# Kernel optimization log

Measured on AMD Instinct MI355X. Metric: run time of the kernel, lower is better.

## Reference

```python
import jax, jax.numpy as jnp
import numpy as np


def setup_inputs() -> dict:
    key = jax.random.key(0)
    k1, k2, k3, k4, k5 = jax.random.split(key, 5)
    B, S, E, U = 32, 2048, 1024, 1024
    last_hidden_state = jax.random.normal(k1, (B, S, E), dtype=jnp.float32)
    attention_mask = jax.random.randint(k2, (B, S), 0, 2, dtype=jnp.int32)
    # ensure at least one valid token per row to avoid all -inf softmax
    attention_mask = attention_mask.at[:, 0].set(1)
    W = jax.random.normal(k3, (U, E), dtype=jnp.float32) * (E ** -0.5)
    Umat = jax.random.normal(k4, (U, E), dtype=jnp.float32) * (E ** -0.5)
    v = jax.random.normal(k5, (1, U), dtype=jnp.float32) * (U ** -0.5)
    return {"last_hidden_state": last_hidden_state, "attention_mask": attention_mask,
            "W": W, "U": Umat, "v": v}


def reference(last_hidden_state, attention_mask, W, U, v):
    # last_hidden_state: [B,S,E]; W,U: [units,E]; v: [1,units]
    Q = jnp.einsum('bse,ue->bsu', last_hidden_state, W)
    K = jnp.einsum('bse,ue->bsu', last_hidden_state, U)
    H = jnp.tanh(Q + K)                                   # [B,S,units]
    E = jnp.einsum('bsu,ou->bso', H, v)                   # [B,S,1]
    neg_inf = jnp.array(-jnp.inf, dtype=E.dtype)
    E = jnp.where(attention_mask[:, :, None] == 0, neg_inf, E)
    alpha = jax.nn.softmax(E, axis=1)                     # softmax over seq dim
    return jnp.sum(alpha * last_hidden_state, axis=1)     # [B,E]
```

## Files before the change

kernel.cpp:

```cpp
#include <hip/hip_runtime.h>
#include <hip/hip_bf16.h>


typedef short bf16x8 __attribute__((ext_vector_type(8)));
typedef float f32x4  __attribute__((ext_vector_type(4)));
typedef unsigned short u16x8 __attribute__((ext_vector_type(8)));

static __device__ __forceinline__ unsigned short f2bf(float f) {
    unsigned int x = __float_as_uint(f);
    unsigned int r = x + 0x7FFFu + ((x >> 16) & 1u);
    return (unsigned short)(r >> 16);
}

static __device__ __forceinline__ float fast_tanh(float x) {
    float e = __builtin_amdgcn_exp2f(x * 2.885390082f);
    float r = __builtin_amdgcn_rcpf(e + 1.0f);
    return __builtin_fmaf(-2.0f, r, 1.0f);
}

__global__ __launch_bounds__(256)
void prep_index(const float* __restrict__ W, const float* __restrict__ U,
                const int* __restrict__ mask,
                unsigned short* __restrict__ wsum,
                float* __restrict__ score, float* __restrict__ out,
                unsigned short* __restrict__ ridx, int* __restrict__ cnt) {
    __shared__ int sc[256];
    int blk = blockIdx.x, t = threadIdx.x;
    if (blk < 1024) {
        int g = blk * 256 + t;
        int i4 = g * 4;
        float4 w = *(const float4*)&W[i4];
        float4 u = *(const float4*)&U[i4];
        ushort4 h;
        h.x = f2bf(w.x + u.x); h.y = f2bf(w.y + u.y);
        h.z = f2bf(w.z + u.z); h.w = f2bf(w.w + u.w);
        *(ushort4*)&wsum[i4] = h;
        if (g < 65536) score[g] = 0.0f;
        if (g < 32768) out[g] = 0.0f;
    } else {
        int b = blk - 1024;
        const int* mrow = mask + b * 2048;
        int m[8], c = 0;
#pragma unroll
        for (int j = 0; j < 8; ++j) { m[j] = mrow[t * 8 + j]; c += (m[j] != 0); }
        sc[t] = c;
        __syncthreads();
        for (int off = 1; off < 256; off <<= 1) {
            int v = (t >= off) ? sc[t - off] : 0;
            __syncthreads();
            sc[t] += v;
            __syncthreads();
        }
        int base = sc[t] - c;
        unsigned short* rb = ridx + b * 2048;
#pragma unroll
        for (int j = 0; j < 8; ++j)
            if (m[j]) rb[base++] = (unsigned short)(t * 8 + j);
        if (t == 255) cnt[b] = sc[255];
    }
}

__global__ __launch_bounds__(256)
void gather_convert(const float* __restrict__ lhs, const unsigned short* __restrict__ ridx,
                    const int* __restrict__ cnt, unsigned short* __restrict__ Ab) {
    int b = blockIdx.y;
    int c = cnt[b];
    int cpad = (c + 127) & ~127;
    int r = blockIdx.x * 4 + (threadIdx.x >> 6);
    int lt = threadIdx.x & 63;
    if (r >= cpad) return;
    unsigned short* dst = Ab + ((size_t)b * 2048 + r) * 1024 + lt * 16;
    if (r < c) {
        int s = ridx[b * 2048 + r];
        const float* src = lhs + ((size_t)b * 2048 + s) * 1024 + lt * 16;
        float4 a0 = *(const float4*)(src + 0);
        float4 a1 = *(const float4*)(src + 4);
        float4 a2 = *(const float4*)(src + 8);
        float4 a3 = *(const float4*)(src + 12);
        u16x8 h0, h1;
        h0[0] = f2bf(a0.x); h0[1] = f2bf(a0.y); h0[2] = f2bf(a0.z); h0[3] = f2bf(a0.w);
        h0[4] = f2bf(a1.x); h0[5] = f2bf(a1.y); h0[6] = f2bf(a1.z); h0[7] = f2bf(a1.w);
        h1[0] = f2bf(a2.x); h1[1] = f2bf(a2.y); h1[2] = f2bf(a2.z); h1[3] = f2bf(a2.w);
        h1[4] = f2bf(a3.x); h1[5] = f2bf(a3.y); h1[6] = f2bf(a3.z); h1[7] = f2bf(a3.w);
        *(u16x8*)(dst + 0) = h0;
        *(u16x8*)(dst + 8) = h1;
    } else {
        u16x8 z = (u16x8){0,0,0,0,0,0,0,0};
        *(u16x8*)(dst + 0) = z;
        *(u16x8*)(dst + 8) = z;
    }
}

__global__ __launch_bounds__(256)
void score_gemm_bf16(const unsigned short* __restrict__ Ab,
                     const unsigned short* __restrict__ Bw,
                     const float* __restrict__ v, const int* __restrict__ cnt,
                     float* __restrict__ score) {
    const int K = 1024;
    __shared__ __align__(16) unsigned short As[128 * 64];
    __shared__ __align__(16) unsigned short Bs[128 * 64];

    const int bid    = (int)blockIdx.x;
    const int group  = bid >> 6;
    const int mt     = (group << 3) + (bid & 7);
    const int nI     = (bid >> 3) & 7;
    const int b      = mt >> 4;
    const int lm0    = (mt & 15) << 7;
    const int c      = cnt[b];
    if (lm0 >= ((c + 127) & ~127)) return;
    const int m0     = (b << 11) + lm0;
    const int n0     = nI << 7;

    const int t    = threadIdx.x;
    const int lane = t & 63;
    const int wave = t >> 6;
    const int wm   = (wave & 1) * 64;
    const int wn   = (wave >> 1) * 64;
    const int ml   = lane & 15;
    const int q    = lane >> 4;
    const int xorv = ml & 7;

    f32x4 acc[4][4];
#pragma unroll
    for (int i = 0; i < 4; ++i)
#pragma unroll
        for (int j = 0; j < 4; ++j)
            acc[i][j] = (f32x4){0.f, 0.f, 0.f, 0.f};

    const unsigned short* gA[4];
    const unsigned short* gB[4];
    unsigned short* lA[4];
    unsigned short* lB[4];
#pragma unroll
    for (int p = 0; p < 4; ++p) {
        int l   = p * 256 + wave * 64 + lane;
        int row = l >> 3;
        int kc  = (l & 7) ^ (row & 7);
        gA[p] = Ab + (size_t)(m0 + row) * K + kc * 8;
        gB[p] = Bw + (size_t)(n0 + row) * K + kc * 8;
        lA[p] = &As[(p * 4 + wave) * 512];
        lB[p] = &Bs[(p * 4 + wave) * 512];
    }

    for (int kk = 0; kk < K; kk += 64) {
#pragma unroll
        for (int p = 0; p < 4; ++p) {
            __builtin_amdgcn_global_load_lds((const __attribute__((address_space(1))) unsigned int*)gA[p],
                                             (__attribute__((address_space(3))) unsigned int*)lA[p], 16, 0, 0);
            __builtin_amdgcn_global_load_lds((const __attribute__((address_space(1))) unsigned int*)gB[p],
                                             (__attribute__((address_space(3))) unsigned int*)lB[p], 16, 0, 0);
            gA[p] += 64; gB[p] += 64;
        }
        __syncthreads();

#pragma unroll
        for (int s = 0; s < 2; ++s) {
            const int koff = ((s * 4 + q) ^ xorv) * 8;
            bf16x8 af[4], bf[4];
#pragma unroll
            for (int i = 0; i < 4; ++i)
                af[i] = *(const bf16x8*)&As[(wm + i * 16 + ml) * 64 + koff];
#pragma unroll
            for (int j = 0; j < 4; ++j)
                bf[j] = *(const bf16x8*)&Bs[(wn + j * 16 + ml) * 64 + koff];
#pragma unroll
            for (int i = 0; i < 4; ++i)
#pragma unroll
                for (int j = 0; j < 4; ++j)
                    acc[i][j] = __builtin_amdgcn_mfma_f32_16x16x32_bf16(af[i], bf[j], acc[i][j], 0, 0, 0);
        }
        __syncthreads();
    }

    float vw[4];
#pragma unroll
    for (int j = 0; j < 4; ++j)
        vw[j] = v[n0 + wn + j * 16 + ml];

#pragma unroll
    for (int i = 0; i < 4; ++i) {
#pragma unroll
        for (int r = 0; r < 4; ++r) {
            float val = 0.f;
#pragma unroll
            for (int j = 0; j < 4; ++j)
                val += fast_tanh(acc[i][j][r]) * vw[j];
#pragma unroll
            for (int off = 8; off > 0; off >>= 1)
                val += __shfl_xor(val, off, 64);
            if (ml == 0)
                atomicAdd(&score[m0 + wm + i * 16 + q * 4 + r], val);
        }
    }
}

__global__ __launch_bounds__(256)
void softmax_compact(const float* __restrict__ score, const int* __restrict__ cnt,
                     float* __restrict__ alphac) {
    int b = blockIdx.x, t = threadIdx.x;
    int c = cnt[b];
    __shared__ float red[8];
    float sc[8];
    float mx = -1e30f;
#pragma unroll
    for (int i = 0; i < 8; ++i) {
        int k = i * 256 + t;
        sc[i] = (k < c) ? score[b * 2048 + k] : -1e30f;
        mx = fmaxf(mx, sc[i]);
    }
#pragma unroll
    for (int off = 32; off > 0; off >>= 1)
        mx = fmaxf(mx, __shfl_xor(mx, off, 64));
    if ((t & 63) == 0) red[t >> 6] = mx;
    __syncthreads();
    mx = fmaxf(fmaxf(red[0], red[1]), fmaxf(red[2], red[3]));
    float e[8], sum = 0.f;
#pragma unroll
    for (int i = 0; i < 8; ++i) {
        int k = i * 256 + t;
        e[i] = (k < c) ? __expf(sc[i] - mx) : 0.f;
        sum += e[i];
    }
#pragma unroll
    for (int off = 32; off > 0; off >>= 1)
        sum += __shfl_xor(sum, off, 64);
    if ((t & 63) == 0) red[4 + (t >> 6)] = sum;
    __syncthreads();
    float inv = 1.0f / (red[4] + red[5] + red[6] + red[7]);
#pragma unroll
    for (int i = 0; i < 8; ++i) {
        int k = i * 256 + t;
        if (k < c) alphac[b * 2048 + k] = e[i] * inv;
    }
}

__global__ __launch_bounds__(256)
void wsum_bf16(const unsigned short* __restrict__ Ab, const float* __restrict__ alphac,
               const int* __restrict__ cnt, float* __restrict__ out) {
    int b   = blockIdx.x >> 4;
    int seg = blockIdx.x & 15;
    int t   = threadIdx.x;
    int c   = cnt[b];
    int per = (c + 15) >> 4;
    int s0  = seg * per;
    int s1  = min(s0 + per, c);
    const float* ap = alphac + b * 2048;
    const unsigned short* base = Ab + (size_t)b * 2048 * 1024 + t * 4;
    float a0 = 0.f, a1 = 0.f, a2 = 0.f, a3 = 0.f;
    for (int s = s0; s < s1; ++s) {
        float a = ap[s];
        ushort4 h = *(const ushort4*)(base + (size_t)s * 1024);
        a0 = __builtin_fmaf(a, __uint_as_float((unsigned)h.x << 16), a0);
        a1 = __builtin_fmaf(a, __uint_as_float((unsigned)h.y << 16), a1);
        a2 = __builtin_fmaf(a, __uint_as_float((unsigned)h.z << 16), a2);
        a3 = __builtin_fmaf(a, __uint_as_float((unsigned)h.w << 16), a3);
    }
    float* o = out + b * 1024 + t * 4;
    atomicAdd(o + 0, a0);
    atomicAdd(o + 1, a1);
    atomicAdd(o + 2, a2);
    atomicAdd(o + 3, a3);
}

#define LDSS 40
__global__ __launch_bounds__(256)
void score_gemm_f32stage(const float* __restrict__ A, const unsigned short* __restrict__ Bw,
                         const float* __restrict__ v, float* __restrict__ score) {
    const int K = 1024;
    __shared__ __align__(16) unsigned short As[128][LDSS];
    __shared__ __align__(16) unsigned short Bs[128][LDSS];
    const int n0 = (int)blockIdx.x * 128;
    const int m0 = (int)blockIdx.y * 128;
    const int t = threadIdx.x, lane = t & 63, wave = t >> 6;
    const int wm = (wave & 1) * 64, wn = (wave >> 1) * 64;
    const int ml = lane & 15, q = lane >> 4;
    f32x4 acc[4][4];
#pragma unroll
    for (int i = 0; i < 4; ++i)
#pragma unroll
        for (int j = 0; j < 4; ++j) acc[i][j] = (f32x4){0.f,0.f,0.f,0.f};
    const int sr = t >> 3, sc = (t & 7) * 4;
    for (int kk = 0; kk < K; kk += 32) {
#pragma unroll
        for (int p = 0; p < 4; ++p) {
            int r = sr + p * 32;
            float4 va = *(const float4*)&A[(size_t)(m0 + r) * K + kk + sc];
            ushort4 h; h.x = f2bf(va.x); h.y = f2bf(va.y); h.z = f2bf(va.z); h.w = f2bf(va.w);
            *(ushort4*)&As[r][sc] = h;
            ushort4 vb = *(const ushort4*)&Bw[(size_t)(n0 + r) * K + kk + sc];
            *(ushort4*)&Bs[r][sc] = vb;
        }
        __syncthreads();
        bf16x8 af[4], bf[4];
#pragma unroll
        for (int i = 0; i < 4; ++i) af[i] = *(const bf16x8*)&As[wm + i * 16 + ml][q * 8];
#pragma unroll
        for (int j = 0; j < 4; ++j) bf[j] = *(const bf16x8*)&Bs[wn + j * 16 + ml][q * 8];
#pragma unroll
        for (int i = 0; i < 4; ++i)
#pragma unroll
            for (int j = 0; j < 4; ++j)
                acc[i][j] = __builtin_amdgcn_mfma_f32_16x16x32_bf16(af[i], bf[j], acc[i][j], 0, 0, 0);
        __syncthreads();
    }
    float vw[4];
#pragma unroll
    for (int j = 0; j < 4; ++j) vw[j] = v[n0 + wn + j * 16 + ml];
#pragma unroll
    for (int i = 0; i < 4; ++i)
#pragma unroll
        for (int r = 0; r < 4; ++r) {
            float val = 0.f;
#pragma unroll
            for (int j = 0; j < 4; ++j) val += fast_tanh(acc[i][j][r]) * vw[j];
#pragma unroll
            for (int off = 8; off > 0; off >>= 1) val += __shfl_xor(val, off, 64);
            if (ml == 0) atomicAdd(&score[m0 + wm + i * 16 + q * 4 + r], val);
        }
}

__global__ __launch_bounds__(256)
void softmax_kernel(const float* __restrict__ score, const int* __restrict__ mask,
                    float* __restrict__ alpha) {
    const int S = 2048;
    int b = blockIdx.x, t = threadIdx.x;
    __shared__ float red[8];
    float sc[8]; int vd[8];
    float mx = -1e30f;
#pragma unroll
    for (int i = 0; i < 8; ++i) {
        int s = i * 256 + t;
        vd[i] = mask[b * S + s];
        sc[i] = score[b * S + s];
        if (vd[i]) mx = fmaxf(mx, sc[i]);
    }
#pragma unroll
    for (int off = 32; off > 0; off >>= 1)
        mx = fmaxf(mx, __shfl_xor(mx, off, 64));
    if ((t & 63) == 0) red[t >> 6] = mx;
    __syncthreads();
    mx = fmaxf(fmaxf(red[0], red[1]), fmaxf(red[2], red[3]));
    float e[8]; float sum = 0.f;
#pragma unroll
    for (int i = 0; i < 8; ++i) {
        e[i] = vd[i] ? __expf(sc[i] - mx) : 0.f;
        sum += e[i];
    }
#pragma unroll
    for (int off = 32; off > 0; off >>= 1)
        sum += __shfl_xor(sum, off, 64);
    if ((t & 63) == 0) red[4 + (t >> 6)] = sum;
    __syncthreads();
    float inv = 1.0f / (red[4] + red[5] + red[6] + red[7]);
#pragma unroll
    for (int i = 0; i < 8; ++i)
        alpha[b * S + i * 256 + t] = e[i] * inv;
}

__global__ __launch_bounds__(256)
void wsum_kernel(const float* __restrict__ lhs, const float* __restrict__ alpha,
                 float* __restrict__ out) {
    const int S = 2048, E = 1024;
    int b = blockIdx.x >> 6;
    int seg = blockIdx.x & 63;
    int t = threadIdx.x;
    int s0 = seg * 32;
    const float* base = lhs + ((size_t)b * S + s0) * E + t * 4;
    const float* ap = alpha + b * S + s0;
    float4 acc = {0.f, 0.f, 0.f, 0.f};
#pragma unroll 4
    for (int s = 0; s < 32; ++s) {
        float a = ap[s];
        if (a != 0.f) {
            float4 x = *(const float4*)(base + (size_t)s * E);
            acc.x += a * x.x; acc.y += a * x.y; acc.z += a * x.z; acc.w += a * x.w;
        }
    }
    float* o = out + b * E + t * 4;
    atomicAdd(o + 0, acc.x);
    atomicAdd(o + 1, acc.y);
    atomicAdd(o + 2, acc.z);
    atomicAdd(o + 3, acc.w);
}

extern "C" void kernel_launch(void* const* d_in, const int* in_sizes, int n_in,
                              void* d_out, int out_size, void* d_ws, size_t ws_size,
                              hipStream_t stream) {
    const float* lhs  = (const float*)d_in[0];
    const int*   mask = (const int*)d_in[1];
    const float* W    = (const float*)d_in[2];
    const float* Um   = (const float*)d_in[3];
    const float* v    = (const float*)d_in[4];
    float* out = (float*)d_out;

    char* ws = (char*)d_ws;
    unsigned short* wsum  = (unsigned short*)ws;
    float* score          = (float*)(ws + 2048u * 1024u);
    float* alphac         = (float*)(ws + 2304u * 1024u);
    unsigned short* ridx  = (unsigned short*)(ws + 2560u * 1024u);
    int* cnt              = (int*)(ws + 2688u * 1024u);
    unsigned short* Ab    = (unsigned short*)(ws + 2816u * 1024u);
    const size_t need = 2816ull * 1024ull + 131072ull * 1024ull;

    prep_index<<<1056, 256, 0, stream>>>(W, Um, mask, wsum, score, out, ridx, cnt);
    if (ws_size >= need) {
        dim3 gg(512, 32);
        gather_convert<<<gg, 256, 0, stream>>>(lhs, ridx, cnt, Ab);
        score_gemm_bf16<<<4096, 256, 0, stream>>>(Ab, wsum, v, cnt, score);
        softmax_compact<<<32, 256, 0, stream>>>(score, cnt, alphac);
        wsum_bf16<<<512, 256, 0, stream>>>(Ab, alphac, cnt, out);
    } else {
        dim3 g1(8, 512);
        score_gemm_f32stage<<<g1, 256, 0, stream>>>(lhs, wsum, v, score);
        softmax_kernel<<<32, 256, 0, stream>>>(score, mask, alphac);
        wsum_kernel<<<2048, 256, 0, stream>>>(lhs, alphac, out);
    }
}
```

Before: 514.1 us.

## Load GEMM B operand directly from pre-packed global layout into registers

The prep kernel now also writes the summed W+U weights in a k-chunk-major packed layout, so each lane's 8-element bf16 fragment is contiguous. The score GEMM drops the B tile from LDS and reads B fragments straight from global memory (L2-resident) into registers, halving LDS traffic and staging work per k-step. This adds an extra 2 MB workspace buffer and exposes global-load latency inside the MFMA loop without explicit prefetching.

```diff
diff --git a/kernel.cpp b/kernel.cpp
--- a/kernel.cpp
+++ b/kernel.cpp
@@ -21,7 +21,7 @@
 __global__ __launch_bounds__(256)
 void prep_index(const float* __restrict__ W, const float* __restrict__ U,
                 const int* __restrict__ mask,
-                unsigned short* __restrict__ wsum,
+                unsigned short* __restrict__ Bt, unsigned short* __restrict__ wsumrm,
                 float* __restrict__ score, float* __restrict__ out,
                 unsigned short* __restrict__ ridx, int* __restrict__ cnt) {
     __shared__ int sc[256];
@@ -34,7 +34,10 @@
         ushort4 h;
         h.x = f2bf(w.x + u.x); h.y = f2bf(w.y + u.y);
         h.z = f2bf(w.z + u.z); h.w = f2bf(w.w + u.w);
-        *(ushort4*)&wsum[i4] = h;
+        *(ushort4*)&wsumrm[i4] = h;
+        int n  = i4 >> 10;
+        int k0 = i4 & 1023;
+        *(ushort4*)&Bt[(size_t)(k0 >> 3) * 8192 + n * 8 + (k0 & 7)] = h;
         if (g < 65536) score[g] = 0.0f;
         if (g < 32768) out[g] = 0.0f;
     } else {
@@ -92,13 +95,12 @@
 }
 
 __global__ __launch_bounds__(256)
-void score_gemm_bf16(const unsigned short* __restrict__ Ab,
-                     const unsigned short* __restrict__ Bw,
-                     const float* __restrict__ v, const int* __restrict__ cnt,
-                     float* __restrict__ score) {
+void score_gemm_v3(const unsigned short* __restrict__ Ab,
+                   const unsigned short* __restrict__ Bt,
+                   const float* __restrict__ v, const int* __restrict__ cnt,
+                   float* __restrict__ score) {
     const int K = 1024;
     __shared__ __align__(16) unsigned short As[128 * 64];
-    __shared__ __align__(16) unsigned short Bs[128 * 64];
 
     const int bid    = (int)blockIdx.x;
     const int group  = bid >> 6;
@@ -128,47 +130,50 @@
             acc[i][j] = (f32x4){0.f, 0.f, 0.f, 0.f};
 
     const unsigned short* gA[4];
-    const unsigned short* gB[4];
     unsigned short* lA[4];
-    unsigned short* lB[4];
 #pragma unroll
     for (int p = 0; p < 4; ++p) {
         int l   = p * 256 + wave * 64 + lane;
         int row = l >> 3;
         int kc  = (l & 7) ^ (row & 7);
         gA[p] = Ab + (size_t)(m0 + row) * K + kc * 8;
-        gB[p] = Bw + (size_t)(n0 + row) * K + kc * 8;
         lA[p] = &As[(p * 4 + wave) * 512];
-        lB[p] = &Bs[(p * 4 + wave) * 512];
-    }
+    }
+
+    const unsigned short* bp[4];
+#pragma unroll
+    for (int j = 0; j < 4; ++j)
+        bp[j] = Bt + (size_t)q * 8192 + (n0 + wn + j * 16 + ml) * 8;
 
     for (int kk = 0; kk < K; kk += 64) {
 #pragma unroll
         for (int p = 0; p < 4; ++p) {
             __builtin_amdgcn_global_load_lds((const __attribute__((address_space(1))) unsigned int*)gA[p],
                                              (__attribute__((address_space(3))) unsigned int*)lA[p], 16, 0, 0);
-            __builtin_amdgcn_global_load_lds((const __attribute__((address_space(1))) unsigned int*)gB[p],
-                                             (__attribute__((address_space(3))) unsigned int*)lB[p], 16, 0, 0);
-            gA[p] += 64; gB[p] += 64;
+            gA[p] += 64;
         }
         __syncthreads();
 
 #pragma unroll
         for (int s = 0; s < 2; ++s) {
+            bf16x8 bf[4];
+#pragma unroll
+            for (int j = 0; j < 4; ++j)
+                bf[j] = *(const bf16x8*)(bp[j] + (size_t)s * 32768);
             const int koff = ((s * 4 + q) ^ xorv) * 8;
-            bf16x8 af[4], bf[4];
+            bf16x8 af[4];
 #pragma unroll
             for (int i = 0; i < 4; ++i)
                 af[i] = *(const bf16x8*)&As[(wm + i * 16 + ml) * 64 + koff];
 #pragma unroll
-            for (int j = 0; j < 4; ++j)
-                bf[j] = *(const bf16x8*)&Bs[(wn + j * 16 + ml) * 64 + koff];
-#pragma unroll
             for (int i = 0; i < 4; ++i)
 #pragma unroll
                 for (int j = 0; j < 4; ++j)
                     acc[i][j] = __builtin_amdgcn_mfma_f32_16x16x32_bf16(af[i], bf[j], acc[i][j], 0, 0, 0);
         }
+#pragma unroll
+        for (int j = 0; j < 4; ++j)
+            bp[j] += 65536;
         __syncthreads();
     }
 
@@ -394,24 +399,25 @@
     float* out = (float*)d_out;
 
     char* ws = (char*)d_ws;
-    unsigned short* wsum  = (unsigned short*)ws;
-    float* score          = (float*)(ws + 2048u * 1024u);
-    float* alphac         = (float*)(ws + 2304u * 1024u);
-    unsigned short* ridx  = (unsigned short*)(ws + 2560u * 1024u);
-    int* cnt              = (int*)(ws + 2688u * 1024u);
-    unsigned short* Ab    = (unsigned short*)(ws + 2816u * 1024u);
-    const size_t need = 2816ull * 1024ull + 131072ull * 1024ull;
-
-    prep_index<<<1056, 256, 0, stream>>>(W, Um, mask, wsum, score, out, ridx, cnt);
+    unsigned short* Bt     = (unsigned short*)ws;
+    unsigned short* wsumrm = (unsigned short*)(ws + 2048u * 1024u);
+    float* score           = (float*)(ws + 4096u * 1024u);
+    float* alphac          = (float*)(ws + 4352u * 1024u);
+    unsigned short* ridx   = (unsigned short*)(ws + 4608u * 1024u);
+    int* cnt               = (int*)(ws + 4736u * 1024u);
+    unsigned short* Ab     = (unsigned short*)(ws + 5120u * 1024u);
+    const size_t need = 5120ull * 1024ull + 131072ull * 1024ull;
+
+    prep_index<<<1056, 256, 0, stream>>>(W, Um, mask, Bt, wsumrm, score, out, ridx, cnt);
     if (ws_size >= need) {
         dim3 gg(512, 32);
         gather_convert<<<gg, 256, 0, stream>>>(lhs, ridx, cnt, Ab);
-        score_gemm_bf16<<<4096, 256, 0, stream>>>(Ab, wsum, v, cnt, score);
+        score_gemm_v3<<<4096, 256, 0, stream>>>(Ab, Bt, v, cnt, score);
         softmax_compact<<<32, 256, 0, stream>>>(score, cnt, alphac);
         wsum_bf16<<<512, 256, 0, stream>>>(Ab, alphac, cnt, out);
     } else {
         dim3 g1(8, 512);
-        score_gemm_f32stage<<<g1, 256, 0, stream>>>(lhs, wsum, v, score);
+        score_gemm_f32stage<<<g1, 256, 0, stream>>>(lhs, wsumrm, v, score);
         softmax_kernel<<<32, 256, 0, stream>>>(score, mask, alphac);
         wsum_kernel<<<2048, 256, 0, stream>>>(lhs, alphac, out);
     }
```

After: 499.0 us. 1.03x faster.
